# Kernel optimization log

Hardware: AMD Instinct MI355X
Metric: run time of the kernel (lower is better)

## Reference

```python
import jax, jax.numpy as jnp
import numpy as np

B, NX, NY, D_FEAT, CTX, S, T = 64, 32, 32, 1024, 512, 32, 4
N = NX * NY


def build_adjacency_matrix(nx, ny):
    # 4-neighborhood grid adjacency with self loops (faithful to original loop)
    adj = np.eye(nx * ny, dtype=np.float32)
    row = 0
    for i in range(nx):
        for j in range(ny):
            if i > 0:
                adj[row, j + (i - 1) * nx] = 1.0
            if i < nx - 1:
                adj[row, j + (i + 1) * nx] = 1.0
            if j > 0:
                adj[row, j - 1 + i * nx] = 1.0
            if j < ny - 1:
                adj[row, j + 1 + i * nx] = 1.0
            row += 1
    return adj


def setup_inputs() -> dict:
    key = jax.random.key(0)
    ks = jax.random.split(key, 12)
    s = 0.02
    return {
        "images": jax.random.normal(ks[0], (B, N, D_FEAT), jnp.float32),
        "q_encoding": jax.random.normal(ks[1], (B, CTX), jnp.float32),
        "lstm_outputs": jax.random.normal(ks[2], (B, S, CTX), jnp.float32),
        "q_length": jax.random.randint(ks[3], (B,), 1, S + 1, jnp.int32),
        "adj": jnp.asarray(build_adjacency_matrix(NX, NY)),
        "initKB_w": jax.random.normal(ks[4], (CTX, D_FEAT), jnp.float32) * s,
        "initKB_b": jnp.zeros((CTX,), jnp.float32),
        "W_w": jax.random.normal(ks[5], (CTX, 2 * CTX), jnp.float32) * s,
        "W_b": jnp.zeros((CTX,), jnp.float32),
        "qInput_w": jax.random.normal(ks[6], (CTX, CTX), jnp.float32) * s,
        "qInput_b": jnp.zeros((CTX,), jnp.float32),
        "qInputT_w": jax.random.normal(ks[7], (T, CTX, CTX), jnp.float32) * s,
        "qInputT_b": jnp.zeros((T, CTX), jnp.float32),
        "cmd_w": jax.random.normal(ks[8], (1, CTX), jnp.float32) * s,
        "cmd_b": jnp.zeros((1,), jnp.float32),
    }


def reference(images, q_encoding, lstm_outputs, q_length, adj,
              initKB_w, initKB_b, W_w, W_b, qInput_w, qInput_b,
              qInputT_w, qInputT_b, cmd_w, cmd_b) -> jnp.ndarray:
    n_iter = qInputT_w.shape[0]
    seq = lstm_outputs.shape[1]
    # loc_init: images [B,N,D_FEAT] -> x_loc [B,N,CTX]
    x_loc = jnp.einsum("bnd,cd->bnc", images, initKB_w) + initKB_b
    # shared first command layer (cfg.CMD_INPUT_ACT = elu)
    q1 = jax.nn.elu(q_encoding @ qInput_w.T + qInput_b)  # [B,CTX]
    valid = jnp.arange(seq)[None, :] < q_length[:, None]  # [B,S]
    for t in range(n_iter):
        # extract_textual_command
        q_cmd = q1 @ qInputT_w[t].T + qInputT_b[t]  # [B,CTX]
        raw_att = jnp.einsum("bsd,d->bs", q_cmd[:, None, :] * lstm_outputs, cmd_w[0]) + cmd_b[0]
        raw_att = jnp.where(valid, raw_att, -1e30)
        att = jax.nn.softmax(raw_att, axis=-1)  # [B,S]
        cmd = jnp.einsum("bs,bsd->bd", att, lstm_outputs)  # [B,CTX]
        # propagate_message: concat + linear, then dense adjacency matmul
        cmd_tiled = jnp.broadcast_to(cmd[:, None, :], x_loc.shape)
        support = jnp.concatenate([x_loc, cmd_tiled], axis=-1) @ W_w.T + W_b  # [B,N,CTX]
        x_new = jnp.einsum("nm,bmd->bnd", adj, support)  # [B,N,CTX]
        x_loc = jax.nn.elu(x_new) if t < n_iter - 1 else x_new
    return x_loc
```

## Files before the change

### kernel.cpp

```cpp
#include <hip/hip_runtime.h>
#include <hip/hip_bf16.h>
#include <math.h>

#define NB 64
#define NNODES 1024
#define CTXD 512
#define SEQL 32

typedef __attribute__((ext_vector_type(8))) short short8;
typedef __attribute__((ext_vector_type(4))) float floatx4;

__device__ __forceinline__ float bf2f(unsigned short u) {
  union { unsigned int i; float f; } v; v.i = ((unsigned int)u) << 16; return v.f;
}
__device__ __forceinline__ unsigned short f2bf(float f) {
  union { float f; unsigned int i; } v; v.f = f;
  unsigned int r = v.i + 0x7fffu + ((v.i >> 16) & 1u);
  return (unsigned short)(r >> 16);
}
__device__ __forceinline__ float elu1(float x) { return x > 0.f ? x : expm1f(x); }

__device__ __forceinline__ void gload16(const void* g, void* l) {
  __builtin_amdgcn_global_load_lds((const __attribute__((address_space(1))) void*)g,
                                   (__attribute__((address_space(3))) void*)l, 16, 0, 0);
}

__global__ __launch_bounds__(256) void pack_k(const float* __restrict__ kbw,
                                              const float* __restrict__ Ww,
                                              const float* __restrict__ qiw,
                                              const float* __restrict__ qtw,
                                              unsigned short* __restrict__ kb_bf,
                                              unsigned short* __restrict__ w1_bf,
                                              float* __restrict__ qiT,
                                              float* __restrict__ qTT,
                                              float* __restrict__ w2T) {
  int idx = blockIdx.x * 256 + threadIdx.x;
  if (idx < 524288) {
    kb_bf[idx] = f2bf(kbw[idx]);
  } else if (idx < 786432) {
    int o = idx - 524288;
    w1_bf[o] = f2bf(Ww[(o >> 9) * 1024 + (o & 511)]);
  } else if (idx < 1048576) {
    int o = idx - 786432;
    int k = o >> 9, c = o & 511;
    qiT[o] = qiw[c * 512 + k];
  } else if (idx < 2097152) {
    int o = idx - 1048576;
    int t = o >> 18, r = o & 262143;
    int k = r >> 9, c = r & 511;
    qTT[o] = qtw[((size_t)t * 512 + c) * 512 + k];
  } else {
    int o = idx - 2097152;
    int k = o >> 9, c = o & 511;
    w2T[o] = Ww[c * 1024 + 512 + k];
  }
}

__global__ __launch_bounds__(512) void q1_k(const float* __restrict__ q_enc,
                                            const float* __restrict__ qiT,
                                            const float* __restrict__ qInput_b,
                                            float* __restrict__ q1) {
  int b = blockIdx.x, c = threadIdx.x;
  __shared__ float qes[512];
  qes[c] = q_enc[b * 512 + c];
  __syncthreads();
  float a0 = qInput_b[c], a1 = 0.f, a2 = 0.f, a3 = 0.f;
#pragma unroll 4
  for (int k = 0; k < 512; k += 4) {
    a0 += qes[k] * qiT[k * 512 + c];
    a1 += qes[k + 1] * qiT[(k + 1) * 512 + c];
    a2 += qes[k + 2] * qiT[(k + 2) * 512 + c];
    a3 += qes[k + 3] * qiT[(k + 3) * 512 + c];
  }
  q1[b * 512 + c] = elu1(a0 + a1 + a2 + a3);
}

__global__ __launch_bounds__(512) void cmdt_k(
    const float* __restrict__ q1, const float* __restrict__ lstm,
    const int* __restrict__ q_len,
    const float* __restrict__ qTT, const float* __restrict__ qT_b,
    const float* __restrict__ cmd_w, const float* __restrict__ cmd_b,
    const float* __restrict__ w2T, const float* __restrict__ W_b,
    float* __restrict__ bias2) {
  int b = blockIdx.x & 63;
  int t = blockIdx.x >> 6;
  int c = threadIdx.x;
  __shared__ float q1s[512];
  __shared__ float us[512];
  __shared__ float red[512];
  __shared__ float atts[32];
  __shared__ float cmds[512];

  q1s[c] = q1[b * 512 + c];
  __syncthreads();

  const float* wt = qTT + (size_t)t * 262144;
  float a0 = qT_b[t * 512 + c], a1 = 0.f, a2 = 0.f, a3 = 0.f;
#pragma unroll 4
  for (int k = 0; k < 512; k += 4) {
    a0 += q1s[k] * wt[k * 512 + c];
    a1 += q1s[k + 1] * wt[(k + 1) * 512 + c];
    a2 += q1s[k + 2] * wt[(k + 2) * 512 + c];
    a3 += q1s[k + 3] * wt[(k + 3) * 512 + c];
  }
  us[c] = (a0 + a1 + a2 + a3) * cmd_w[c];
  __syncthreads();

  const float* lstmb = lstm + (size_t)b * SEQL * 512;
  {
    int s = c >> 4, u = c & 15;
    float p = 0.f;
    const float* lr = lstmb + s * 512;
    for (int r = u; r < 512; r += 16) p += us[r] * lr[r];
    red[c] = p;
  }
  __syncthreads();
  if (c < 32) {
    float raw = cmd_b[0];
    for (int u = 0; u < 16; u++) raw += red[c * 16 + u];
    raw = (c < q_len[b]) ? raw : -1e30f;
    float mx = raw;
    for (int off = 16; off; off >>= 1) mx = fmaxf(mx, __shfl_xor(mx, off, 32));
    float e = expf(raw - mx);
    float sm = e;
    for (int off = 16; off; off >>= 1) sm += __shfl_xor(sm, off, 32);
    atts[c] = e / sm;
  }
  __syncthreads();
  float cd = 0.f;
#pragma unroll
  for (int s = 0; s < 32; s++) cd += atts[s] * lstmb[s * 512 + c];
  cmds[c] = cd;
  __syncthreads();

  float b0 = W_b[c], b1 = 0.f, b2 = 0.f, b3 = 0.f;
#pragma unroll 4
  for (int k = 0; k < 512; k += 4) {
    b0 += cmds[k] * w2T[k * 512 + c];
    b1 += cmds[k + 1] * w2T[(k + 1) * 512 + c];
    b2 += cmds[k + 2] * w2T[(k + 2) * 512 + c];
    b3 += cmds[k + 3] * w2T[(k + 3) * 512 + c];
  }
  bias2[((size_t)(t * 64 + b)) * 512 + c] = b0 + b1 + b2 + b3;
}

__global__ __launch_bounds__(256) void stencil_k(const unsigned short* __restrict__ x,
                                                 unsigned short* __restrict__ y) {
  int g = blockIdx.x * 256 + threadIdx.x;
  int v = g & 63;
  int n = (g >> 6) & 1023;
  int b = g >> 16;
  size_t base = ((((size_t)b << 10) + n) << 9) + v * 8;
  const unsigned short* p = x + base;
  float acc[8];
  short8 s = *(const short8*)p;
#pragma unroll
  for (int j = 0; j < 8; j++) acc[j] = bf2f((unsigned short)s[j]);
  int i = n >> 5, jj = n & 31;
  if (i > 0) {
    short8 t = *(const short8*)(p - 32 * 512);
#pragma unroll
    for (int j = 0; j < 8; j++) acc[j] += bf2f((unsigned short)t[j]);
  }
  if (i < 31) {
    short8 t = *(const short8*)(p + 32 * 512);
#pragma unroll
    for (int j = 0; j < 8; j++) acc[j] += bf2f((unsigned short)t[j]);
  }
  if (jj > 0) {
    short8 t = *(const short8*)(p - 512);
#pragma unroll
    for (int j = 0; j < 8; j++) acc[j] += bf2f((unsigned short)t[j]);
  }
  if (jj < 31) {
    short8 t = *(const short8*)(p + 512);
#pragma unroll
    for (int j = 0; j < 8; j++) acc[j] += bf2f((unsigned short)t[j]);
  }
  short8 o;
#pragma unroll
  for (int j = 0; j < 8; j++) o[j] = (short)f2bf(acc[j]);
  *(short8*)(y + base) = o;
}

template <int AF32, int MODE>
__global__ __launch_bounds__(256) void gemm_bt(
    const void* __restrict__ Ap, int lda,
    const unsigned short* __restrict__ Bw, int ldb, int K,
    const float* __restrict__ cbias, const float* __restrict__ bias2,
    void* __restrict__ Cp) {
  __shared__ __align__(128) unsigned short As[128 * 64];
  __shared__ __align__(128) unsigned short Bs[128 * 64];

  const int tid = threadIdx.x;
  const int lane = tid & 63;
  const int wave = tid >> 6;
  const int wr = (wave >> 1) * 64;
  const int wc = (wave & 1) * 64;
  const int lr = lane & 15;
  const int lk = lane >> 4;
  const int lr7 = lr & 7;

  int bid = blockIdx.x;
  int cpx = gridDim.x >> 3;
  int wg = (bid & 7) * cpx + (bid >> 3);
  int mtile = wg >> 2;
  int ntile = wg & 3;
  const size_t rowBase = (size_t)mtile * 128;
  const int colBase = ntile * 128;

  floatx4 acc[4][4];
#pragma unroll
  for (int m = 0; m < 4; m++)
#pragma unroll
    for (int n = 0; n < 4; n++) acc[m][n] = {0.f, 0.f, 0.f, 0.f};

  for (int k0 = 0; k0 < K; k0 += 64) {
    __syncthreads();
    if constexpr (AF32) {
      const float* A = (const float*)Ap;
#pragma unroll
      for (int j = 0; j < 4; j++) {
        int g = j * 256 + tid;
        int r = g >> 3, s = g & 7;
        const float* src = A + (rowBase + r) * (size_t)lda + k0 + s * 8;
        floatx4 v0 = *(const floatx4*)src;
        floatx4 v1 = *(const floatx4*)(src + 4);
        short8 t;
#pragma unroll
        for (int e = 0; e < 4; e++) {
          __hip_bfloat16 h0 = __float2bfloat16(v0[e]);
          __hip_bfloat16 h1 = __float2bfloat16(v1[e]);
          t[e] = (short)*reinterpret_cast<unsigned short*>(&h0);
          t[e + 4] = (short)*reinterpret_cast<unsigned short*>(&h1);
        }
        *(short8*)((char*)As + r * 128 + ((s ^ (r & 7)) << 4)) = t;
      }
    } else {
      const unsigned short* A = (const unsigned short*)Ap;
#pragma unroll
      for (int j = 0; j < 4; j++) {
        int g = j * 256 + tid;
        int r = g >> 3, u = g & 7;
        gload16(A + (rowBase + r) * (size_t)lda + k0 + ((u ^ (r & 7)) << 3),
                (char*)As + g * 16);
      }
    }
#pragma unroll
    for (int j = 0; j < 4; j++) {
      int g = j * 256 + tid;
      int r = g >> 3, u = g & 7;
      gload16(Bw + (size_t)(colBase + r) * ldb + k0 + ((u ^ (r & 7)) << 3),
              (char*)Bs + g * 16);
    }
    __syncthreads();

#pragma unroll
    for (int kk = 0; kk < 2; kk++) {
      const int ub = ((kk << 2) + lk) ^ lr7;
      short8 a[4], b[4];
#pragma unroll
      for (int m = 0; m < 4; m++)
        a[m] = *(const short8*)((const char*)As + (wr + m * 16 + lr) * 128 + (ub << 4));
#pragma unroll
      for (int n = 0; n < 4; n++)
        b[n] = *(const short8*)((const char*)Bs + (wc + n * 16 + lr) * 128 + (ub << 4));
#pragma unroll
      for (int m = 0; m < 4; m++)
#pragma unroll
        for (int n = 0; n < 4; n++)
          acc[m][n] = __builtin_amdgcn_mfma_f32_16x16x32_bf16(a[m], b[n], acc[m][n], 0, 0, 0);
    }
  }

#pragma unroll
  for (int m = 0; m < 4; m++) {
#pragma unroll
    for (int q = 0; q < 4; q++) {
      size_t grow = rowBase + wr + m * 16 + lk * 4 + q;
      float degf = 0.f;
      const float* b2 = nullptr;
      if constexpr (MODE != 0) {
        int nsp = (int)(grow & 1023);
        int ii = nsp >> 5, jj = nsp & 31;
        degf = (float)(1 + (ii > 0) + (ii < 31) + (jj > 0) + (jj < 31));
        b2 = bias2 + (grow >> 10) * CTXD;
      }
#pragma unroll
      for (int n = 0; n < 4; n++) {
        int gcol = colBase + wc + n * 16 + lr;
        float v = acc[m][n][q];
        if constexpr (MODE == 0) v += cbias[gcol];
        else v += degf * b2[gcol];
        if constexpr (MODE == 1) v = elu1(v);
        if constexpr (MODE == 2) ((float*)Cp)[grow * CTXD + gcol] = v;
        else ((unsigned short*)Cp)[grow * CTXD + gcol] = f2bf(v);
      }
    }
  }
}

extern "C" void kernel_launch(void* const* d_in, const int* in_sizes, int n_in,
                              void* d_out, int out_size, void* d_ws, size_t ws_size,
                              hipStream_t stream) {
  const float* images   = (const float*)d_in[0];
  const float* q_enc    = (const float*)d_in[1];
  const float* lstm     = (const float*)d_in[2];
  const int*   q_len    = (const int*)d_in[3];
  const float* initKB_w = (const float*)d_in[5];
  const float* initKB_b = (const float*)d_in[6];
  const float* W_w      = (const float*)d_in[7];
  const float* W_b      = (const float*)d_in[8];
  const float* qInput_w = (const float*)d_in[9];
  const float* qInput_b = (const float*)d_in[10];
  const float* qT_w     = (const float*)d_in[11];
  const float* qT_b     = (const float*)d_in[12];
  const float* cmd_w    = (const float*)d_in[13];
  const float* cmd_b    = (const float*)d_in[14];

  char* ws = (char*)d_ws;
  unsigned short* y     = (unsigned short*)ws;
  float*          qiT   = (float*)ws;
  float*          qTT   = (float*)(ws + 1048576);
  float*          w2T   = (float*)(ws + 5242880);
  unsigned short* kb_bf = (unsigned short*)(ws + 67108864);
  unsigned short* w1_bf = (unsigned short*)(ws + 68157440);
  float*          bias2 = (float*)(ws + 68681728);
  float*          q1    = (float*)(ws + 69206016);
  unsigned short* xloc  = (unsigned short*)d_out;

  pack_k<<<9216, 256, 0, stream>>>(initKB_w, W_w, qInput_w, qT_w,
                                   kb_bf, w1_bf, qiT, qTT, w2T);
  q1_k<<<64, 512, 0, stream>>>(q_enc, qiT, qInput_b, q1);
  cmdt_k<<<256, 512, 0, stream>>>(q1, lstm, q_len, qTT, qT_b, cmd_w, cmd_b,
                                  w2T, W_b, bias2);

  gemm_bt<1, 0><<<2048, 256, 0, stream>>>(images, 1024, kb_bf, 1024, 1024,
                                          initKB_b, nullptr, xloc);

  for (int t = 0; t < 4; t++) {
    stencil_k<<<16384, 256, 0, stream>>>(xloc, y);
    if (t < 3)
      gemm_bt<0, 1><<<2048, 256, 0, stream>>>(y, 512, w1_bf, 512, 512,
                                              nullptr, bias2 + (size_t)t * 64 * 512, xloc);
    else
      gemm_bt<0, 2><<<2048, 256, 0, stream>>>(y, 512, w1_bf, 512, 512,
                                              nullptr, bias2 + (size_t)t * 64 * 512, d_out);
  }
}
```

Before: 544.3 us.

## Add 256x256-tile double-buffered MFMA GEMM for per-iteration message projection

Adds a new bf16 MFMA GEMM kernel with 256x256 output tiles, 512 threads, and double-buffered LDS staging via direct global-to-LDS loads with XOR swizzle. It replaces the previous gemm_bt for the four per-iteration W projections. It also remaps block IDs so neighbouring blocks share data in the same XCD/cache. The larger tile raises operand reuse and cuts the number of blocks, but it uses 128 KB of LDS and many accumulators, which can limit occupancy. With only 512 blocks, it also risks a tail effect on 256 CUs.

```diff
diff --git a/kernel.cpp b/kernel.cpp
--- a/kernel.cpp
+++ b/kernel.cpp
@@ -300,6 +300,116 @@
   }
 }
 
+template <int MODE>
+__global__ __launch_bounds__(512, 2) void gemm256(
+    const unsigned short* __restrict__ A, int lda,
+    const unsigned short* __restrict__ Bw, int ldb, int K,
+    const float* __restrict__ bias2, void* __restrict__ Cp) {
+  __shared__ __align__(128) unsigned short As[2][256 * 64];
+  __shared__ __align__(128) unsigned short Bs[2][256 * 64];
+
+  const int tid = threadIdx.x;
+  const int lane = tid & 63;
+  const int wave = tid >> 6;
+  const int wm = wave >> 2;
+  const int wn = wave & 3;
+  const int lr = lane & 15;
+  const int lk = lane >> 4;
+  const int lr7 = lr & 7;
+
+  int bid = blockIdx.x;
+  int cpx = gridDim.x >> 3;
+  int wg = (bid & 7) * cpx + (bid >> 3);
+  const size_t rowBase = (size_t)(wg >> 1) * 256;
+  const int colBase = (wg & 1) * 256;
+
+  floatx4 acc[8][4];
+#pragma unroll
+  for (int m = 0; m < 8; m++)
+#pragma unroll
+    for (int n = 0; n < 4; n++) acc[m][n] = {0.f, 0.f, 0.f, 0.f};
+
+  auto stage = [&](int buf, int kt) {
+    const int kbase = kt * 64;
+#pragma unroll
+    for (int j = 0; j < 4; j++) {
+      int g = j * 512 + tid;
+      int r = g >> 3, u = g & 7;
+      gload16(A + (rowBase + r) * (size_t)lda + kbase + ((u ^ (r & 7)) << 3),
+              (char*)&As[buf][0] + g * 16);
+    }
+#pragma unroll
+    for (int j = 0; j < 4; j++) {
+      int g = j * 512 + tid;
+      int r = g >> 3, u = g & 7;
+      gload16(Bw + (size_t)(colBase + r) * ldb + kbase + ((u ^ (r & 7)) << 3),
+              (char*)&Bs[buf][0] + g * 16);
+    }
+  };
+
+  const int NT = K >> 6;
+  stage(0, 0);
+  stage(1, 1);
+
+  for (int kt = 0; kt < NT; kt++) {
+    const int cur = kt & 1;
+    if (kt < NT - 1) {
+      asm volatile("s_waitcnt vmcnt(8)" ::: "memory");
+    } else {
+      asm volatile("s_waitcnt vmcnt(0)" ::: "memory");
+    }
+    __builtin_amdgcn_s_barrier();
+    __builtin_amdgcn_sched_barrier(0);
+
+    const unsigned short* Ab = &As[cur][0];
+    const unsigned short* Bb = &Bs[cur][0];
+#pragma unroll
+    for (int kk = 0; kk < 2; kk++) {
+      const int ub = ((kk << 2) + lk) ^ lr7;
+      short8 a[8], b[4];
+#pragma unroll
+      for (int m = 0; m < 8; m++)
+        a[m] = *(const short8*)((const char*)Ab + (wm * 128 + m * 16 + lr) * 128 + (ub << 4));
+#pragma unroll
+      for (int n = 0; n < 4; n++)
+        b[n] = *(const short8*)((const char*)Bb + (wn * 64 + n * 16 + lr) * 128 + (ub << 4));
+#pragma unroll
+      for (int m = 0; m < 8; m++)
+#pragma unroll
+        for (int n = 0; n < 4; n++)
+          acc[m][n] = __builtin_amdgcn_mfma_f32_16x16x32_bf16(a[m], b[n], acc[m][n], 0, 0, 0);
+    }
+
+    if (kt + 2 < NT) {
+      __builtin_amdgcn_sched_barrier(0);
+      __builtin_amdgcn_s_barrier();
+      stage(cur, kt + 2);
+    }
+  }
+
+#pragma unroll
+  for (int m = 0; m < 8; m++) {
+#pragma unroll
+    for (int q = 0; q < 4; q++) {
+      size_t grow = rowBase + wm * 128 + m * 16 + lk * 4 + q;
+      int nsp = (int)(grow & 1023);
+      int ii = nsp >> 5, jj = nsp & 31;
+      float degf = (float)(1 + (ii > 0) + (ii < 31) + (jj > 0) + (jj < 31));
+      const float* b2 = bias2 + (grow >> 10) * CTXD;
+#pragma unroll
+      for (int n = 0; n < 4; n++) {
+        int gcol = colBase + wn * 64 + n * 16 + lr;
+        float v = acc[m][n][q] + degf * b2[gcol];
+        if constexpr (MODE == 1) {
+          ((unsigned short*)Cp)[grow * CTXD + gcol] = f2bf(elu1(v));
+        } else {
+          ((float*)Cp)[grow * CTXD + gcol] = v;
+        }
+      }
+    }
+  }
+}
+
 extern "C" void kernel_launch(void* const* d_in, const int* in_sizes, int n_in,
                               void* d_out, int out_size, void* d_ws, size_t ws_size,
                               hipStream_t stream) {
@@ -341,10 +451,10 @@
   for (int t = 0; t < 4; t++) {
     stencil_k<<<16384, 256, 0, stream>>>(xloc, y);
     if (t < 3)
-      gemm_bt<0, 1><<<2048, 256, 0, stream>>>(y, 512, w1_bf, 512, 512,
-                                              nullptr, bias2 + (size_t)t * 64 * 512, xloc);
+      gemm256<1><<<512, 512, 0, stream>>>(y, 512, w1_bf, 512, 512,
+                                          bias2 + (size_t)t * 64 * 512, xloc);
     else
-      gemm_bt<0, 2><<<2048, 256, 0, stream>>>(y, 512, w1_bf, 512, 512,
-                                              nullptr, bias2 + (size_t)t * 64 * 512, d_out);
-  }
-}
+      gemm256<2><<<512, 512, 0, stream>>>(y, 512, w1_bf, 512, 512,
+                                          bias2 + (size_t)t * 64 * 512, d_out);
+  }
+}
```

New measurement: 563.2 us. +3.5%, slower.

## Fuse grid stencil into GEMM A-tile load and retile to 64x256

Applied to the files above, without the earlier changes.

Removes the separate stencil kernel and instead sums the 4-neighbour rows while loading each A tile into shared memory inside the GEMM, ping-ponging between two buffers. The GEMM tile changes from 128x128 to 64 rows by 256 columns, so each block covers half of the 512 output columns, with a launch-bounds occupancy hint added. This drops a full write and read of the intermediate activation per iteration and four kernel launches. In exchange, the neighbour rows are re-read redundantly by the two column tiles, and A loading becomes synchronous register loads instead of direct-to-LDS loads.

```diff
diff --git a/kernel.cpp b/kernel.cpp
--- a/kernel.cpp
+++ b/kernel.cpp
@@ -144,59 +144,18 @@
   bias2[((size_t)(t * 64 + b)) * 512 + c] = b0 + b1 + b2 + b3;
 }
 
-__global__ __launch_bounds__(256) void stencil_k(const unsigned short* __restrict__ x,
-                                                 unsigned short* __restrict__ y) {
-  int g = blockIdx.x * 256 + threadIdx.x;
-  int v = g & 63;
-  int n = (g >> 6) & 1023;
-  int b = g >> 16;
-  size_t base = ((((size_t)b << 10) + n) << 9) + v * 8;
-  const unsigned short* p = x + base;
-  float acc[8];
-  short8 s = *(const short8*)p;
-#pragma unroll
-  for (int j = 0; j < 8; j++) acc[j] = bf2f((unsigned short)s[j]);
-  int i = n >> 5, jj = n & 31;
-  if (i > 0) {
-    short8 t = *(const short8*)(p - 32 * 512);
-#pragma unroll
-    for (int j = 0; j < 8; j++) acc[j] += bf2f((unsigned short)t[j]);
-  }
-  if (i < 31) {
-    short8 t = *(const short8*)(p + 32 * 512);
-#pragma unroll
-    for (int j = 0; j < 8; j++) acc[j] += bf2f((unsigned short)t[j]);
-  }
-  if (jj > 0) {
-    short8 t = *(const short8*)(p - 512);
-#pragma unroll
-    for (int j = 0; j < 8; j++) acc[j] += bf2f((unsigned short)t[j]);
-  }
-  if (jj < 31) {
-    short8 t = *(const short8*)(p + 512);
-#pragma unroll
-    for (int j = 0; j < 8; j++) acc[j] += bf2f((unsigned short)t[j]);
-  }
-  short8 o;
-#pragma unroll
-  for (int j = 0; j < 8; j++) o[j] = (short)f2bf(acc[j]);
-  *(short8*)(y + base) = o;
-}
-
-template <int AF32, int MODE>
-__global__ __launch_bounds__(256) void gemm_bt(
+template <int AMODE, int MODE>
+__global__ __launch_bounds__(256, 3) void tgemm(
     const void* __restrict__ Ap, int lda,
     const unsigned short* __restrict__ Bw, int ldb, int K,
     const float* __restrict__ cbias, const float* __restrict__ bias2,
     void* __restrict__ Cp) {
-  __shared__ __align__(128) unsigned short As[128 * 64];
-  __shared__ __align__(128) unsigned short Bs[128 * 64];
+  __shared__ __align__(128) unsigned short As[64 * 64];
+  __shared__ __align__(128) unsigned short Bs[256 * 64];
 
   const int tid = threadIdx.x;
   const int lane = tid & 63;
-  const int wave = tid >> 6;
-  const int wr = (wave >> 1) * 64;
-  const int wc = (wave & 1) * 64;
+  const int wn = tid >> 6;
   const int lr = lane & 15;
   const int lk = lane >> 4;
   const int lr7 = lr & 7;
@@ -204,10 +163,8 @@
   int bid = blockIdx.x;
   int cpx = gridDim.x >> 3;
   int wg = (bid & 7) * cpx + (bid >> 3);
-  int mtile = wg >> 2;
-  int ntile = wg & 3;
-  const size_t rowBase = (size_t)mtile * 128;
-  const int colBase = ntile * 128;
+  const size_t rowBase = (size_t)(wg >> 1) * 64;
+  const int colBase = (wg & 1) * 256;
 
   floatx4 acc[4][4];
 #pragma unroll
@@ -217,37 +174,65 @@
 
   for (int k0 = 0; k0 < K; k0 += 64) {
     __syncthreads();
-    if constexpr (AF32) {
-      const float* A = (const float*)Ap;
-#pragma unroll
-      for (int j = 0; j < 4; j++) {
+    if constexpr (AMODE == 0) {
+      const float* Af = (const float*)Ap;
+#pragma unroll
+      for (int j = 0; j < 2; j++) {
         int g = j * 256 + tid;
-        int r = g >> 3, s = g & 7;
-        const float* src = A + (rowBase + r) * (size_t)lda + k0 + s * 8;
+        int r = g >> 3, u = g & 7;
+        const float* src = Af + (rowBase + r) * (size_t)lda + k0 + u * 8;
         floatx4 v0 = *(const floatx4*)src;
         floatx4 v1 = *(const floatx4*)(src + 4);
         short8 t;
 #pragma unroll
         for (int e = 0; e < 4; e++) {
-          __hip_bfloat16 h0 = __float2bfloat16(v0[e]);
-          __hip_bfloat16 h1 = __float2bfloat16(v1[e]);
-          t[e] = (short)*reinterpret_cast<unsigned short*>(&h0);
-          t[e + 4] = (short)*reinterpret_cast<unsigned short*>(&h1);
-        }
-        *(short8*)((char*)As + r * 128 + ((s ^ (r & 7)) << 4)) = t;
+          t[e] = (short)f2bf(v0[e]);
+          t[e + 4] = (short)f2bf(v1[e]);
+        }
+        *(short8*)((char*)As + r * 128 + ((u ^ (r & 7)) << 4)) = t;
       }
     } else {
-      const unsigned short* A = (const unsigned short*)Ap;
-#pragma unroll
-      for (int j = 0; j < 4; j++) {
+      const unsigned short* X = (const unsigned short*)Ap;
+#pragma unroll
+      for (int j = 0; j < 2; j++) {
         int g = j * 256 + tid;
         int r = g >> 3, u = g & 7;
-        gload16(A + (rowBase + r) * (size_t)lda + k0 + ((u ^ (r & 7)) << 3),
-                (char*)As + g * 16);
+        size_t R = rowBase + r;
+        int n = (int)(R & 1023);
+        int gi = n >> 5, gj = n & 31;
+        const unsigned short* p = X + R * 512 + k0 + u * 8;
+        short8 c = *(const short8*)p;
+        float s[8];
+#pragma unroll
+        for (int e = 0; e < 8; e++) s[e] = bf2f((unsigned short)c[e]);
+        if (gi > 0) {
+          short8 t = *(const short8*)(p - 32 * 512);
+#pragma unroll
+          for (int e = 0; e < 8; e++) s[e] += bf2f((unsigned short)t[e]);
+        }
+        if (gi < 31) {
+          short8 t = *(const short8*)(p + 32 * 512);
+#pragma unroll
+          for (int e = 0; e < 8; e++) s[e] += bf2f((unsigned short)t[e]);
+        }
+        if (gj > 0) {
+          short8 t = *(const short8*)(p - 512);
+#pragma unroll
+          for (int e = 0; e < 8; e++) s[e] += bf2f((unsigned short)t[e]);
+        }
+        if (gj < 31) {
+          short8 t = *(const short8*)(p + 512);
+#pragma unroll
+          for (int e = 0; e < 8; e++) s[e] += bf2f((unsigned short)t[e]);
+        }
+        short8 o;
+#pragma unroll
+        for (int e = 0; e < 8; e++) o[e] = (short)f2bf(s[e]);
+        *(short8*)((char*)As + r * 128 + ((u ^ (r & 7)) << 4)) = o;
       }
     }
 #pragma unroll
-    for (int j = 0; j < 4; j++) {
+    for (int j = 0; j < 8; j++) {
       int g = j * 256 + tid;
       int r = g >> 3, u = g & 7;
       gload16(Bw + (size_t)(colBase + r) * ldb + k0 + ((u ^ (r & 7)) << 3),
@@ -261,10 +246,10 @@
       short8 a[4], b[4];
 #pragma unroll
       for (int m = 0; m < 4; m++)
-        a[m] = *(const short8*)((const char*)As + (wr + m * 16 + lr) * 128 + (ub << 4));
+        a[m] = *(const short8*)((const char*)As + (m * 16 + lr) * 128 + (ub << 4));
 #pragma unroll
       for (int n = 0; n < 4; n++)
-        b[n] = *(const short8*)((const char*)Bs + (wc + n * 16 + lr) * 128 + (ub << 4));
+        b[n] = *(const short8*)((const char*)Bs + (wn * 64 + n * 16 + lr) * 128 + (ub << 4));
 #pragma unroll
       for (int m = 0; m < 4; m++)
 #pragma unroll
@@ -277,7 +262,7 @@
   for (int m = 0; m < 4; m++) {
 #pragma unroll
     for (int q = 0; q < 4; q++) {
-      size_t grow = rowBase + wr + m * 16 + lk * 4 + q;
+      size_t grow = rowBase + m * 16 + lk * 4 + q;
       float degf = 0.f;
       const float* b2 = nullptr;
       if constexpr (MODE != 0) {
@@ -288,7 +273,7 @@
       }
 #pragma unroll
       for (int n = 0; n < 4; n++) {
-        int gcol = colBase + wc + n * 16 + lr;
+        int gcol = colBase + wn * 64 + n * 16 + lr;
         float v = acc[m][n][q];
         if constexpr (MODE == 0) v += cbias[gcol];
         else v += degf * b2[gcol];
@@ -319,7 +304,7 @@
   const float* cmd_b    = (const float*)d_in[14];
 
   char* ws = (char*)d_ws;
-  unsigned short* y     = (unsigned short*)ws;
+  unsigned short* X1    = (unsigned short*)ws;
   float*          qiT   = (float*)ws;
   float*          qTT   = (float*)(ws + 1048576);
   float*          w2T   = (float*)(ws + 5242880);
@@ -327,7 +312,7 @@
   unsigned short* w1_bf = (unsigned short*)(ws + 68157440);
   float*          bias2 = (float*)(ws + 68681728);
   float*          q1    = (float*)(ws + 69206016);
-  unsigned short* xloc  = (unsigned short*)d_out;
+  unsigned short* X0    = (unsigned short*)d_out;
 
   pack_k<<<9216, 256, 0, stream>>>(initKB_w, W_w, qInput_w, qT_w,
                                    kb_bf, w1_bf, qiT, qTT, w2T);
@@ -335,16 +320,15 @@
   cmdt_k<<<256, 512, 0, stream>>>(q1, lstm, q_len, qTT, qT_b, cmd_w, cmd_b,
                                   w2T, W_b, bias2);
 
-  gemm_bt<1, 0><<<2048, 256, 0, stream>>>(images, 1024, kb_bf, 1024, 1024,
-                                          initKB_b, nullptr, xloc);
-
-  for (int t = 0; t < 4; t++) {
-    stencil_k<<<16384, 256, 0, stream>>>(xloc, y);
-    if (t < 3)
-      gemm_bt<0, 1><<<2048, 256, 0, stream>>>(y, 512, w1_bf, 512, 512,
-                                              nullptr, bias2 + (size_t)t * 64 * 512, xloc);
-    else
-      gemm_bt<0, 2><<<2048, 256, 0, stream>>>(y, 512, w1_bf, 512, 512,
-                                              nullptr, bias2 + (size_t)t * 64 * 512, d_out);
-  }
-}
+  tgemm<0, 0><<<2048, 256, 0, stream>>>(images, 1024, kb_bf, 1024, 1024,
+                                        initKB_b, nullptr, X0);
+
+  tgemm<1, 1><<<2048, 256, 0, stream>>>(X0, 512, w1_bf, 512, 512,
+                                        nullptr, bias2 + 0 * 32768, X1);
+  tgemm<1, 1><<<2048, 256, 0, stream>>>(X1, 512, w1_bf, 512, 512,
+                                        nullptr, bias2 + 1 * 32768, X0);
+  tgemm<1, 1><<<2048, 256, 0, stream>>>(X0, 512, w1_bf, 512, 512,
+                                        nullptr, bias2 + 2 * 32768, X1);
+  tgemm<1, 2><<<2048, 256, 0, stream>>>(X1, 512, w1_bf, 512, 512,
+                                        nullptr, bias2 + 3 * 32768, d_out);
+}
```

New measurement: 531.7 us. -2.3%, faster.
